# Kernel optimization log

Measured on AMD Instinct MI355X. Metric: run time of the kernel, lower is better.

## Reference

```python
import jax, jax.numpy as jnp
import numpy as np

B, SQ, SKV = 4, 4096, 1024
QDIM, CDIM = 1024, 768
HEADS, DHEAD = 16, 64
INNER = HEADS * DHEAD


def setup_inputs() -> dict:
    key = jax.random.key(0)
    ks = jax.random.split(key, 7)
    s = 0.02
    return {
        "x": jax.random.normal(ks[0], (B, SQ, QDIM), dtype=jnp.float32),
        "context": jax.random.normal(ks[1], (B, SKV, CDIM), dtype=jnp.float32),
        "Wq": jax.random.normal(ks[2], (QDIM, INNER), dtype=jnp.float32) * s,
        "Wk": jax.random.normal(ks[3], (CDIM, INNER), dtype=jnp.float32) * s,
        "Wv": jax.random.normal(ks[4], (CDIM, INNER), dtype=jnp.float32) * s,
        "Wo": jax.random.normal(ks[5], (INNER, QDIM), dtype=jnp.float32) * s,
        "bo": jnp.zeros((QDIM,), dtype=jnp.float32),
    }


def reference(x, context, Wq, Wk, Wv, Wo, bo):
    # QKV projections (no bias, matching bias=False Linear layers)
    q = x @ Wq          # [B, SQ, INNER]
    k = context @ Wk    # [B, SKV, INNER]
    v = context @ Wv    # [B, SKV, INNER]

    # split heads: b s (h d) -> b h s d
    def split_heads(t, s):
        return t.reshape(B, s, HEADS, DHEAD).transpose(0, 2, 1, 3)

    qh = split_heads(q, SQ)
    kh = split_heads(k, SKV)
    vh = split_heads(v, SKV)

    scale = DHEAD ** -0.5  # attention_basic default scale
    sim = jnp.einsum('bhqd,bhkd->bhqk', qh, kh) * scale  # [B,H,SQ,SKV]
    attn = jax.nn.softmax(sim, axis=-1)
    out = jnp.einsum('bhqk,bhkd->bhqd', attn, vh)        # [B,H,SQ,DHEAD]
    out = out.transpose(0, 2, 1, 3).reshape(B, SQ, INNER)

    # output projection (Linear with bias); dropout p=0 -> identity
    return out @ Wo + bo
```

## Files before the change

kernel.cpp:

```cpp
#include <hip/hip_runtime.h>


typedef unsigned short u16;
typedef unsigned int u32;
typedef __bf16 bf16x8 __attribute__((ext_vector_type(8)));
typedef float float4v __attribute__((ext_vector_type(4)));
typedef _Float16 half4 __attribute__((ext_vector_type(4)));
typedef _Float16 half2v __attribute__((ext_vector_type(2)));
typedef __attribute__((address_space(1))) void as1_void;
typedef __attribute__((address_space(3))) void as3_void;

__device__ __forceinline__ u16 f2bf(float f) {
  unsigned u = __float_as_uint(f);
  u += 0x7FFF + ((u >> 16) & 1);
  return (u16)(u >> 16);
}

__device__ __forceinline__ void async16(const u16* g, u16* l) {
  __builtin_amdgcn_global_load_lds((as1_void*)(void*)g, (as3_void*)l, 16, 0, 0);
}

#define WAITCNT_VM8 0xF78
#define WAITCNT_VM4 0xF74
#define WAITCNT_VM0 0xF70

__global__ void cvt_kernel(const float* __restrict__ x, u16* __restrict__ xbf,
                           const float* __restrict__ ctx, u16* __restrict__ ctxbf) {
  int i = blockIdx.x * 256 + threadIdx.x;
  const float* in; u16* out; int j;
  if (i < 4194304) { in = x; out = xbf; j = i; }
  else if (i < 4980736) { in = ctx; out = ctxbf; j = i - 4194304; }
  else return;
  float4 v = ((const float4*)in)[j];
  ushort4 o;
  o.x = f2bf(v.x); o.y = f2bf(v.y); o.z = f2bf(v.z); o.w = f2bf(v.w);
  ((ushort4*)out)[j] = o;
}

__global__ void twt_kernel(const float* __restrict__ Wq, const float* __restrict__ Wk,
                           const float* __restrict__ Wv, const float* __restrict__ Wo,
                           u16* __restrict__ WqT, u16* __restrict__ WkT,
                           u16* __restrict__ WvT, u16* __restrict__ WoT) {
  __shared__ u16 t[32][33];
  int z = blockIdx.z;
  const float* W = z == 0 ? Wq : z == 1 ? Wk : z == 2 ? Wv : Wo;
  u16* Wt = z == 0 ? WqT : z == 1 ? WkT : z == 2 ? WvT : WoT;
  int Kd = (z == 1 || z == 2) ? 768 : 1024;
  int k0 = blockIdx.y * 32;
  if (k0 >= Kd) return;
  int tx = threadIdx.x, ty = threadIdx.y;
  int n0 = blockIdx.x * 32;
#pragma unroll
  for (int i = 0; i < 4; i++)
    t[ty + i * 8][tx] = f2bf(W[(size_t)(k0 + ty + i * 8) * 1024 + n0 + tx]);
  __syncthreads();
#pragma unroll
  for (int i = 0; i < 4; i++)
    Wt[(size_t)(n0 + ty + i * 8) * Kd + k0 + tx] = t[tx][ty + i * 8];
}


__device__ __forceinline__ void ld_a4(const u16 (*Lp)[256][8], int rbase, int quad,
                                      int l15, bf16x8 a[4][2]) {
#pragma unroll
  for (int mi = 0; mi < 4; mi++)
#pragma unroll
    for (int ks = 0; ks < 2; ks++)
      a[mi][ks] = *(const bf16x8*)&Lp[ks * 4 + quad][rbase + mi * 16 + l15][0];
}

__device__ __forceinline__ void ld_b2(const u16 (*Lp)[256][8], int rbase, int quad,
                                      int l15, bf16x8 b[2][2]) {
#pragma unroll
  for (int ni = 0; ni < 2; ni++)
#pragma unroll
    for (int ks = 0; ks < 2; ks++)
      b[ni][ks] = *(const bf16x8*)&Lp[ks * 4 + quad][rbase + ni * 16 + l15][0];
}

__device__ __forceinline__ void mm16(bf16x8 a[4][2], bf16x8 b[2][2],
                                     float4v acc[8][4], int mh, int nh) {
  __builtin_amdgcn_s_setprio(1);
#pragma unroll
  for (int mi = 0; mi < 4; mi++)
#pragma unroll
    for (int ni = 0; ni < 2; ni++)
#pragma unroll
      for (int ks = 0; ks < 2; ks++)
        acc[mh * 4 + mi][nh * 2 + ni] = __builtin_amdgcn_mfma_f32_16x16x32_bf16(
            a[mi][ks], b[ni][ks], acc[mh * 4 + mi][nh * 2 + ni], 0, 0, 0);
  __builtin_amdgcn_s_setprio(0);
}

__device__ __forceinline__ void gemm256_core(const u16* __restrict__ A,
                                             const u16* __restrict__ Bt, int K,
                                             int m0, int n0, float4v acc[8][4]) {
  __shared__ __align__(16) u16 L[2][2][8][256][8];
  int tid = threadIdx.x;
  int w = tid >> 6, lane = tid & 63;
  int l15 = lane & 15, quad = lane >> 4;
  int wm = (w >> 2) * 128, wn = (w & 3) * 64;

  int c0 = 2 * w, c1 = 2 * w + 1;
  int kc0 = c0 & 7, mb0 = (c0 >> 3) * 64;
  int kc1 = c1 & 7, mb1 = (c1 >> 3) * 64;
  const u16* pA0 = A + (size_t)(m0 + mb0 + lane) * K + kc0 * 8;
  const u16* pA1 = A + (size_t)(m0 + mb1 + lane) * K + kc1 * 8;
  const u16* pB0 = Bt + (size_t)(n0 + mb0 + lane) * K + kc0 * 8;
  const u16* pB1 = Bt + (size_t)(n0 + mb1 + lane) * K + kc1 * 8;
  size_t hs = (size_t)128 * K;

#define STG_A(buf, t)                                                          \
  do {                                                                         \
    const u16* s0 = pA0 + (size_t)(t) * 64;                                    \
    const u16* s1 = pA1 + (size_t)(t) * 64;                                    \
    async16(s0, &L[buf][0][kc0][mb0][0]);                                      \
    async16(s1, &L[buf][0][kc1][mb1][0]);                                      \
    async16(s0 + hs, &L[buf][0][kc0][128 + mb0][0]);                           \
    async16(s1 + hs, &L[buf][0][kc1][128 + mb1][0]);                           \
  } while (0)
#define STG_B(buf, t)                                                          \
  do {                                                                         \
    const u16* s0 = pB0 + (size_t)(t) * 64;                                    \
    const u16* s1 = pB1 + (size_t)(t) * 64;                                    \
    async16(s0, &L[buf][1][kc0][mb0][0]);                                      \
    async16(s1, &L[buf][1][kc1][mb1][0]);                                      \
    async16(s0 + hs, &L[buf][1][kc0][128 + mb0][0]);                           \
    async16(s1 + hs, &L[buf][1][kc1][128 + mb1][0]);                           \
  } while (0)

  STG_A(0, 0); STG_B(0, 0);
  STG_A(1, 1); STG_B(1, 1);
  __builtin_amdgcn_s_waitcnt(WAITCNT_VM8);
  __builtin_amdgcn_s_barrier();

  bf16x8 a[4][2], b0[2][2], b1[2][2];
  int I = K >> 7;
  for (int i = 0; i < I; ++i) {
    int st = (i + 1 < I);
    ld_a4(L[0][0], wm, quad, l15, a);
    ld_b2(L[0][1], wn, quad, l15, b0);
    if (i > 0) STG_B(1, 2 * i + 1);
    __builtin_amdgcn_s_barrier();
    mm16(a, b0, acc, 0, 0);
    __builtin_amdgcn_s_barrier();
    ld_b2(L[0][1], wn + 32, quad, l15, b1);
    __builtin_amdgcn_s_barrier();
    mm16(a, b1, acc, 0, 1);
    __builtin_amdgcn_s_barrier();
    ld_a4(L[0][0], wm + 64, quad, l15, a);
    __builtin_amdgcn_s_barrier();
    mm16(a, b1, acc, 1, 1);
    __builtin_amdgcn_s_barrier();
    if (st) STG_A(0, 2 * i + 2);
    __builtin_amdgcn_s_barrier();
    mm16(a, b0, acc, 1, 0);
    if (st) __builtin_amdgcn_s_waitcnt(WAITCNT_VM4);
    else    __builtin_amdgcn_s_waitcnt(WAITCNT_VM0);
    __builtin_amdgcn_s_barrier();
    ld_a4(L[1][0], wm, quad, l15, a);
    ld_b2(L[1][1], wn, quad, l15, b0);
    if (st) STG_B(0, 2 * i + 2);
    __builtin_amdgcn_s_barrier();
    mm16(a, b0, acc, 0, 0);
    __builtin_amdgcn_s_barrier();
    ld_b2(L[1][1], wn + 32, quad, l15, b1);
    __builtin_amdgcn_s_barrier();
    mm16(a, b1, acc, 0, 1);
    __builtin_amdgcn_s_barrier();
    ld_a4(L[1][0], wm + 64, quad, l15, a);
    __builtin_amdgcn_s_barrier();
    mm16(a, b1, acc, 1, 1);
    __builtin_amdgcn_s_barrier();
    if (st) STG_A(1, 2 * i + 3);
    __builtin_amdgcn_s_barrier();
    mm16(a, b0, acc, 1, 0);
    if (st) __builtin_amdgcn_s_waitcnt(WAITCNT_VM4);
    __builtin_amdgcn_s_barrier();
  }
#undef STG_A
#undef STG_B
}

__global__ __launch_bounds__(512, 2) void qkv_gemm8(
    const u16* __restrict__ xbf, const u16* __restrict__ ctxbf,
    const u16* __restrict__ WqT, const u16* __restrict__ WkT, const u16* __restrict__ WvT,
    u16* __restrict__ Qb, u16* __restrict__ Kbuf, u16* __restrict__ Vtb, float qscale) {
  int bx = blockIdx.x;
  const u16* A; const u16* Bt; u16* C; int K, mode, m0, n0; float scale;
  if (bx < 256)      { int t = bx;       A = xbf;   Bt = WqT; C = Qb;   K = 1024; mode = 0; scale = qscale; m0 = (t >> 2) * 256; n0 = (t & 3) * 256; }
  else if (bx < 320) { int t = bx - 256; A = ctxbf; Bt = WkT; C = Kbuf; K = 768;  mode = 0; scale = 1.0f;   m0 = (t >> 2) * 256; n0 = (t & 3) * 256; }
  else               { int t = bx - 320; A = ctxbf; Bt = WvT; C = Vtb;  K = 768;  mode = 2; scale = 1.0f;   m0 = (t >> 2) * 256; n0 = (t & 3) * 256; }

  float4v acc[8][4] = {};
  gemm256_core(A, Bt, K, m0, n0, acc);

  int tid = threadIdx.x;
  int w = tid >> 6, lane = tid & 63;
  int l15 = lane & 15, quad = lane >> 4;
  int wm = (w >> 2) * 128, wn = (w & 3) * 64;

  if (mode == 0) {
#pragma unroll
    for (int mi = 0; mi < 8; mi++) {
      int rowb = m0 + wm + mi * 16 + quad * 4;
#pragma unroll
      for (int ni = 0; ni < 4; ni++) {
        int col = n0 + wn + ni * 16 + l15;
#pragma unroll
        for (int r = 0; r < 4; r++)
          C[(size_t)(rowb + r) * 1024 + col] = f2bf(acc[mi][ni][r] * scale);
      }
    }
  } else {
#pragma unroll
    for (int mi = 0; mi < 8; mi++) {
      int rowb = m0 + wm + mi * 16 + quad * 4;
#pragma unroll
      for (int ni = 0; ni < 4; ni++) {
        int col = n0 + wn + ni * 16 + l15;
        int hh = col >> 6, dd = col & 63;
#pragma unroll
        for (int r = 0; r < 4; r++) {
          int rr = rowb + r;
          int b = rr >> 10, skv = rr & 1023;
          _Float16 hv = (_Float16)acc[mi][ni][r];
          C[((((size_t)b * 16 + hh) * 64 + dd) << 10) + skv] = __builtin_bit_cast(u16, hv);
        }
      }
    }
  }
}

__global__ __launch_bounds__(512, 2) void gemm_bt8(
    const u16* __restrict__ A, const u16* __restrict__ Bt,
    float* __restrict__ C, const float* __restrict__ bias) {
  int bx = blockIdx.x;
  int m0 = (bx >> 2) * 256, n0 = (bx & 3) * 256;

  float4v acc[8][4] = {};
  gemm256_core(A, Bt, 1024, m0, n0, acc);

  int tid = threadIdx.x;
  int w = tid >> 6, lane = tid & 63;
  int l15 = lane & 15, quad = lane >> 4;
  int wm = (w >> 2) * 128, wn = (w & 3) * 64;

#pragma unroll
  for (int mi = 0; mi < 8; mi++) {
    int rowb = m0 + wm + mi * 16 + quad * 4;
#pragma unroll
    for (int ni = 0; ni < 4; ni++) {
      int col = n0 + wn + ni * 16 + l15;
      float bv = bias[col];
#pragma unroll
      for (int r = 0; r < 4; r++)
        C[(size_t)(rowb + r) * 1024 + col] = acc[mi][ni][r] + bv;
    }
  }
}

__global__ __launch_bounds__(512, 4) void attn_kernel(
    const u16* __restrict__ Q, const u16* __restrict__ Kb,
    const u16* __restrict__ Vt, u16* __restrict__ Oout) {
  __shared__ __align__(16) u16 lK[2][8192];
  __shared__ __align__(16) u16 lV[2][8192];
  int tid = threadIdx.x, w = tid >> 6, lane = tid & 63;
  int l15 = lane & 15, quad = lane >> 4;
  int bh = blockIdx.y, b = bh >> 4, h = bh & 15;
  int q0 = blockIdx.x * 256 + w * 32;

  const u16* Qbase = Q + ((size_t)(b * 4096 + q0)) * 1024 + h * 64;
  const u16* Kbase = Kb + ((size_t)b << 20) + h * 64;
  const u16* Vbase = Vt + ((size_t)bh << 16);

  bf16x8 qf[2][2];
#pragma unroll
  for (int qt = 0; qt < 2; qt++)
#pragma unroll
    for (int c = 0; c < 2; c++)
      qf[qt][c] = *(const bf16x8*)(Qbase + (size_t)(qt * 16 + l15) * 1024 + c * 32 + quad * 8);

  int kr0 = tid >> 3, kx0 = ((tid & 7) ^ (kr0 & 7)) * 8;
  const u16* ks0 = Kbase + (size_t)kr0 * 1024 + kx0;
  const u16* ks1 = ks0 + (size_t)64 * 1024;
  int vd0 = tid >> 4, vc0 = ((tid & 15) ^ (vd0 & 15)) * 8;
  const u16* vs0 = Vbase + (size_t)vd0 * 1024 + vc0;
  const u16* vs1 = vs0 + (size_t)32 * 1024;
  int kdo0 = w * 512, kdo1 = 4096 + w * 512;

  async16(ks0, &lK[0][kdo0]); async16(ks1, &lK[0][kdo1]);
  async16(vs0, &lV[0][kdo0]); async16(vs1, &lV[0][kdo1]);
  ks0 += 131072; ks1 += 131072;
  vs0 += 128; vs1 += 128;

  float4v o[2][4] = {};
  float4v osum[2] = {};
  const half4 ones = {(_Float16)1.0f, (_Float16)1.0f, (_Float16)1.0f, (_Float16)1.0f};

  int lb = l15 & 7;
  int xk0 = ((0 + quad) ^ lb) * 16 + l15 * 128;
  int xk1 = ((4 + quad) ^ lb) * 16 + l15 * 128;
  int qh = quad >> 1, qo = (quad & 1) * 8;
  int vrow = l15 * 256 + qo;

  for (int it = 0; it < 8; ++it) {
    const char* bK = (const char*)lK + (it & 1) * 16384;
    const char* bV = (const char*)lV + (it & 1) * 16384;
    __syncthreads();
    if (it < 7) {
      int nb = (it + 1) & 1;
      async16(ks0, &lK[nb][kdo0]); async16(ks1, &lK[nb][kdo1]);
      async16(vs0, &lV[nb][kdo0]); async16(vs1, &lV[nb][kdo1]);
      ks0 += 131072; ks1 += 131072;
      vs0 += 128; vs1 += 128;
    }
#pragma unroll
    for (int ss = 0; ss < 8; ss++) {
      int sub = (ss + w) & 7;
      int sb = sub * 2048;
      float4v sv[2] = {{0.f, 0.f, 0.f, 0.f}, {0.f, 0.f, 0.f, 0.f}};
      __builtin_amdgcn_s_setprio(1);
#pragma unroll
      for (int c = 0; c < 2; c++) {
        bf16x8 kf = *(const bf16x8*)(bK + sb + (c ? xk1 : xk0));
#pragma unroll
        for (int qt = 0; qt < 2; qt++)
          sv[qt] = __builtin_amdgcn_mfma_f32_16x16x32_bf16(kf, qf[qt][c], sv[qt], 0, 0, 0);
      }
      __builtin_amdgcn_s_setprio(0);
      half4 pf[2];
#pragma unroll
      for (int qt = 0; qt < 2; qt++) {
        float e0 = exp2f(sv[qt][0]), e1 = exp2f(sv[qt][1]);
        float e2 = exp2f(sv[qt][2]), e3 = exp2f(sv[qt][3]);
        half2v p01 = __builtin_bit_cast(half2v, __builtin_amdgcn_cvt_pkrtz(e0, e1));
        half2v p23 = __builtin_bit_cast(half2v, __builtin_amdgcn_cvt_pkrtz(e2, e3));
        pf[qt] = __builtin_shufflevector(p01, p23, 0, 1, 2, 3);
        osum[qt] = __builtin_amdgcn_mfma_f32_16x16x16f16(ones, pf[qt], osum[qt], 0, 0, 0);
      }
      int vbs = vrow + (((sub * 2 + qh) ^ l15) * 16);
      __builtin_amdgcn_s_setprio(1);
#pragma unroll
      for (int dt = 0; dt < 4; dt++) {
        half4 vf = *(const half4*)(bV + dt * 4096 + vbs);
#pragma unroll
        for (int qt = 0; qt < 2; qt++)
          o[qt][dt] = __builtin_amdgcn_mfma_f32_16x16x16f16(vf, pf[qt], o[qt][dt], 0, 0, 0);
      }
      __builtin_amdgcn_s_setprio(0);
    }
  }

#pragma unroll
  for (int qt = 0; qt < 2; qt++) {
    float inv = 1.0f / osum[qt][0];
    u16* Ob = Oout + ((size_t)(b * 4096 + q0 + qt * 16 + l15)) * 1024 + h * 64 + quad * 4;
#pragma unroll
    for (int dt = 0; dt < 4; dt++) {
      ushort4 pk;
      pk.x = f2bf(o[qt][dt][0] * inv);
      pk.y = f2bf(o[qt][dt][1] * inv);
      pk.z = f2bf(o[qt][dt][2] * inv);
      pk.w = f2bf(o[qt][dt][3] * inv);
      *(ushort4*)(Ob + dt * 16) = pk;
    }
  }
}

extern "C" void kernel_launch(void* const* d_in, const int* in_sizes, int n_in,
                              void* d_out, int out_size, void* d_ws, size_t ws_size,
                              hipStream_t stream) {
  const float* x   = (const float*)d_in[0];
  const float* ctx = (const float*)d_in[1];
  const float* Wq  = (const float*)d_in[2];
  const float* Wk  = (const float*)d_in[3];
  const float* Wv  = (const float*)d_in[4];
  const float* Wo  = (const float*)d_in[5];
  const float* bo  = (const float*)d_in[6];
  float* out = (float*)d_out;

  u16* ws    = (u16*)d_ws;
  u16* xbf   = ws;
  u16* ctxbf = xbf + 16777216;
  u16* WqT   = ctxbf + 3145728;
  u16* WkT   = WqT + 1048576;
  u16* WvT   = WkT + 786432;
  u16* WoT   = WvT + 786432;
  u16* Qb    = WoT + 1048576;
  u16* Kbuf  = Qb + 16777216;
  u16* Vtb   = Kbuf + 4194304;
  if (ws_size < (size_t)48758784 * 2) return;

  cvt_kernel<<<19456, 256, 0, stream>>>(x, xbf, ctx, ctxbf);
  twt_kernel<<<dim3(32, 32, 4), dim3(32, 8), 0, stream>>>(Wq, Wk, Wv, Wo, WqT, WkT, WvT, WoT);
  qkv_gemm8<<<dim3(384), dim3(512), 0, stream>>>(xbf, ctxbf, WqT, WkT, WvT,
                                                 Qb, Kbuf, Vtb, 0.18033688011112042f);
  attn_kernel<<<dim3(16, 64), dim3(512), 0, stream>>>(Qb, Kbuf, Vtb, xbf);
  gemm_bt8<<<dim3(256), dim3(512), 0, stream>>>(xbf, WoT, out, bo);
}
```

Before: 378.3 us.

## Replace 256x256 GEMM tiles with 128x128 triple-buffered tiles and block swizzle

Replaces the 8-wave 256x256 GEMM core, with its two-stage buffering and fine-grained barriers, by a 4-wave 128x128 core using three LDS stages with K=32 slices and one barrier per iteration. Block indices are remapped so that consecutive blocks are spread across XCD-style groups. More, smaller tiles should improve wave-level load balance and occupancy on 256 CUs (1536 and 1024 blocks instead of 384 and 256), at the cost of less operand reuse per tile and more global and LDS traffic. The unpadded [128][32] LDS layout may cause bank conflicts.

```diff
diff --git a/kernel.cpp b/kernel.cpp
--- a/kernel.cpp
+++ b/kernel.cpp
@@ -59,150 +59,86 @@
     Wt[(size_t)(n0 + ty + i * 8) * Kd + k0 + tx] = t[tx][ty + i * 8];
 }
 
-
-__device__ __forceinline__ void ld_a4(const u16 (*Lp)[256][8], int rbase, int quad,
-                                      int l15, bf16x8 a[4][2]) {
-#pragma unroll
-  for (int mi = 0; mi < 4; mi++)
-#pragma unroll
-    for (int ks = 0; ks < 2; ks++)
-      a[mi][ks] = *(const bf16x8*)&Lp[ks * 4 + quad][rbase + mi * 16 + l15][0];
-}
-
-__device__ __forceinline__ void ld_b2(const u16 (*Lp)[256][8], int rbase, int quad,
-                                      int l15, bf16x8 b[2][2]) {
-#pragma unroll
-  for (int ni = 0; ni < 2; ni++)
-#pragma unroll
-    for (int ks = 0; ks < 2; ks++)
-      b[ni][ks] = *(const bf16x8*)&Lp[ks * 4 + quad][rbase + ni * 16 + l15][0];
-}
-
-__device__ __forceinline__ void mm16(bf16x8 a[4][2], bf16x8 b[2][2],
-                                     float4v acc[8][4], int mh, int nh) {
-  __builtin_amdgcn_s_setprio(1);
-#pragma unroll
-  for (int mi = 0; mi < 4; mi++)
-#pragma unroll
-    for (int ni = 0; ni < 2; ni++)
-#pragma unroll
-      for (int ks = 0; ks < 2; ks++)
-        acc[mh * 4 + mi][nh * 2 + ni] = __builtin_amdgcn_mfma_f32_16x16x32_bf16(
-            a[mi][ks], b[ni][ks], acc[mh * 4 + mi][nh * 2 + ni], 0, 0, 0);
-  __builtin_amdgcn_s_setprio(0);
-}
-
-__device__ __forceinline__ void gemm256_core(const u16* __restrict__ A,
+__device__ __forceinline__ void gemm128_core(const u16* __restrict__ A,
                                              const u16* __restrict__ Bt, int K,
-                                             int m0, int n0, float4v acc[8][4]) {
-  __shared__ __align__(16) u16 L[2][2][8][256][8];
+                                             int m0, int n0, float4v acc[4][4]) {
+  __shared__ __align__(16) u16 L[3][2][128][32];
   int tid = threadIdx.x;
   int w = tid >> 6, lane = tid & 63;
   int l15 = lane & 15, quad = lane >> 4;
-  int wm = (w >> 2) * 128, wn = (w & 3) * 64;
-
-  int c0 = 2 * w, c1 = 2 * w + 1;
-  int kc0 = c0 & 7, mb0 = (c0 >> 3) * 64;
-  int kc1 = c1 & 7, mb1 = (c1 >> 3) * 64;
-  const u16* pA0 = A + (size_t)(m0 + mb0 + lane) * K + kc0 * 8;
-  const u16* pA1 = A + (size_t)(m0 + mb1 + lane) * K + kc1 * 8;
-  const u16* pB0 = Bt + (size_t)(n0 + mb0 + lane) * K + kc0 * 8;
-  const u16* pB1 = Bt + (size_t)(n0 + mb1 + lane) * K + kc1 * 8;
-  size_t hs = (size_t)128 * K;
-
-#define STG_A(buf, t)                                                          \
+  int wm = (w >> 1) * 64, wn = (w & 1) * 64;
+
+  const u16* pA = A + (size_t)(m0 + (tid >> 2)) * K + (tid & 3) * 8;
+  const u16* pB = Bt + (size_t)(n0 + (tid >> 2)) * K + (tid & 3) * 8;
+  size_t r64 = (size_t)64 * K;
+  int dofs = tid * 8;
+
+#define STG(buf, t)                                                            \
   do {                                                                         \
-    const u16* s0 = pA0 + (size_t)(t) * 64;                                    \
-    const u16* s1 = pA1 + (size_t)(t) * 64;                                    \
-    async16(s0, &L[buf][0][kc0][mb0][0]);                                      \
-    async16(s1, &L[buf][0][kc1][mb1][0]);                                      \
-    async16(s0 + hs, &L[buf][0][kc0][128 + mb0][0]);                           \
-    async16(s1 + hs, &L[buf][0][kc1][128 + mb1][0]);                           \
+    const u16* sa = pA + (size_t)(t) * 32;                                     \
+    const u16* sb = pB + (size_t)(t) * 32;                                     \
+    async16(sa, &L[buf][0][0][0] + dofs);                                      \
+    async16(sa + r64, &L[buf][0][0][0] + dofs + 2048);                         \
+    async16(sb, &L[buf][1][0][0] + dofs);                                      \
+    async16(sb + r64, &L[buf][1][0][0] + dofs + 2048);                         \
   } while (0)
-#define STG_B(buf, t)                                                          \
-  do {                                                                         \
-    const u16* s0 = pB0 + (size_t)(t) * 64;                                    \
-    const u16* s1 = pB1 + (size_t)(t) * 64;                                    \
-    async16(s0, &L[buf][1][kc0][mb0][0]);                                      \
-    async16(s1, &L[buf][1][kc1][mb1][0]);                                      \
-    async16(s0 + hs, &L[buf][1][kc0][128 + mb0][0]);                           \
-    async16(s1 + hs, &L[buf][1][kc1][128 + mb1][0]);                           \
-  } while (0)
-
-  STG_A(0, 0); STG_B(0, 0);
-  STG_A(1, 1); STG_B(1, 1);
-  __builtin_amdgcn_s_waitcnt(WAITCNT_VM8);
-  __builtin_amdgcn_s_barrier();
-
-  bf16x8 a[4][2], b0[2][2], b1[2][2];
-  int I = K >> 7;
-  for (int i = 0; i < I; ++i) {
-    int st = (i + 1 < I);
-    ld_a4(L[0][0], wm, quad, l15, a);
-    ld_b2(L[0][1], wn, quad, l15, b0);
-    if (i > 0) STG_B(1, 2 * i + 1);
+
+  STG(0, 0);
+  STG(1, 1);
+
+  int niter = K >> 5;
+  int cb = 0;
+  for (int it = 0; it < niter; ++it) {
+    if (it + 1 < niter) __builtin_amdgcn_s_waitcnt(WAITCNT_VM4);
+    else                __builtin_amdgcn_s_waitcnt(WAITCNT_VM0);
     __builtin_amdgcn_s_barrier();
-    mm16(a, b0, acc, 0, 0);
-    __builtin_amdgcn_s_barrier();
-    ld_b2(L[0][1], wn + 32, quad, l15, b1);
-    __builtin_amdgcn_s_barrier();
-    mm16(a, b1, acc, 0, 1);
-    __builtin_amdgcn_s_barrier();
-    ld_a4(L[0][0], wm + 64, quad, l15, a);
-    __builtin_amdgcn_s_barrier();
-    mm16(a, b1, acc, 1, 1);
-    __builtin_amdgcn_s_barrier();
-    if (st) STG_A(0, 2 * i + 2);
-    __builtin_amdgcn_s_barrier();
-    mm16(a, b0, acc, 1, 0);
-    if (st) __builtin_amdgcn_s_waitcnt(WAITCNT_VM4);
-    else    __builtin_amdgcn_s_waitcnt(WAITCNT_VM0);
-    __builtin_amdgcn_s_barrier();
-    ld_a4(L[1][0], wm, quad, l15, a);
-    ld_b2(L[1][1], wn, quad, l15, b0);
-    if (st) STG_B(0, 2 * i + 2);
-    __builtin_amdgcn_s_barrier();
-    mm16(a, b0, acc, 0, 0);
-    __builtin_amdgcn_s_barrier();
-    ld_b2(L[1][1], wn + 32, quad, l15, b1);
-    __builtin_amdgcn_s_barrier();
-    mm16(a, b1, acc, 0, 1);
-    __builtin_amdgcn_s_barrier();
-    ld_a4(L[1][0], wm + 64, quad, l15, a);
-    __builtin_amdgcn_s_barrier();
-    mm16(a, b1, acc, 1, 1);
-    __builtin_amdgcn_s_barrier();
-    if (st) STG_A(1, 2 * i + 3);
-    __builtin_amdgcn_s_barrier();
-    mm16(a, b0, acc, 1, 0);
-    if (st) __builtin_amdgcn_s_waitcnt(WAITCNT_VM4);
-    __builtin_amdgcn_s_barrier();
-  }
-#undef STG_A
-#undef STG_B
-}
-
-__global__ __launch_bounds__(512, 2) void qkv_gemm8(
+    if (it + 2 < niter) {
+      int pb = cb + 2; if (pb >= 3) pb -= 3;
+      STG(pb, it + 2);
+    }
+    const u16* cA = &L[cb][0][0][0];
+    const u16* cB = &L[cb][1][0][0];
+    bf16x8 fa[4], fb[4];
+#pragma unroll
+    for (int mi = 0; mi < 4; mi++)
+      fa[mi] = *(const bf16x8*)&cA[(wm + mi * 16 + l15) * 32 + quad * 8];
+#pragma unroll
+    for (int ni = 0; ni < 4; ni++)
+      fb[ni] = *(const bf16x8*)&cB[(wn + ni * 16 + l15) * 32 + quad * 8];
+    __builtin_amdgcn_s_setprio(1);
+#pragma unroll
+    for (int mi = 0; mi < 4; mi++)
+#pragma unroll
+      for (int ni = 0; ni < 4; ni++)
+        acc[mi][ni] = __builtin_amdgcn_mfma_f32_16x16x32_bf16(fa[mi], fb[ni], acc[mi][ni], 0, 0, 0);
+    __builtin_amdgcn_s_setprio(0);
+    cb = (cb + 1 == 3) ? 0 : cb + 1;
+  }
+#undef STG
+}
+
+__global__ __launch_bounds__(256, 3) void qkv_gemm128(
     const u16* __restrict__ xbf, const u16* __restrict__ ctxbf,
     const u16* __restrict__ WqT, const u16* __restrict__ WkT, const u16* __restrict__ WvT,
     u16* __restrict__ Qb, u16* __restrict__ Kbuf, u16* __restrict__ Vtb, float qscale) {
-  int bx = blockIdx.x;
+  int bx0 = blockIdx.x;
+  int bx = (bx0 & 7) * 192 + (bx0 >> 3);
   const u16* A; const u16* Bt; u16* C; int K, mode, m0, n0; float scale;
-  if (bx < 256)      { int t = bx;       A = xbf;   Bt = WqT; C = Qb;   K = 1024; mode = 0; scale = qscale; m0 = (t >> 2) * 256; n0 = (t & 3) * 256; }
-  else if (bx < 320) { int t = bx - 256; A = ctxbf; Bt = WkT; C = Kbuf; K = 768;  mode = 0; scale = 1.0f;   m0 = (t >> 2) * 256; n0 = (t & 3) * 256; }
-  else               { int t = bx - 320; A = ctxbf; Bt = WvT; C = Vtb;  K = 768;  mode = 2; scale = 1.0f;   m0 = (t >> 2) * 256; n0 = (t & 3) * 256; }
-
-  float4v acc[8][4] = {};
-  gemm256_core(A, Bt, K, m0, n0, acc);
+  if (bx < 1024)      { int t = bx;        A = xbf;   Bt = WqT; C = Qb;   K = 1024; mode = 0; scale = qscale; m0 = (t >> 3) * 128; n0 = (t & 7) * 128; }
+  else if (bx < 1280) { int t = bx - 1024; A = ctxbf; Bt = WkT; C = Kbuf; K = 768;  mode = 0; scale = 1.0f;   m0 = (t >> 3) * 128; n0 = (t & 7) * 128; }
+  else                { int t = bx - 1280; A = ctxbf; Bt = WvT; C = Vtb;  K = 768;  mode = 2; scale = 1.0f;   m0 = (t >> 3) * 128; n0 = (t & 7) * 128; }
+
+  float4v acc[4][4] = {};
+  gemm128_core(A, Bt, K, m0, n0, acc);
 
   int tid = threadIdx.x;
   int w = tid >> 6, lane = tid & 63;
   int l15 = lane & 15, quad = lane >> 4;
-  int wm = (w >> 2) * 128, wn = (w & 3) * 64;
+  int wm = (w >> 1) * 64, wn = (w & 1) * 64;
 
   if (mode == 0) {
 #pragma unroll
-    for (int mi = 0; mi < 8; mi++) {
+    for (int mi = 0; mi < 4; mi++) {
       int rowb = m0 + wm + mi * 16 + quad * 4;
 #pragma unroll
       for (int ni = 0; ni < 4; ni++) {
@@ -214,7 +150,7 @@
     }
   } else {
 #pragma unroll
-    for (int mi = 0; mi < 8; mi++) {
+    for (int mi = 0; mi < 4; mi++) {
       int rowb = m0 + wm + mi * 16 + quad * 4;
 #pragma unroll
       for (int ni = 0; ni < 4; ni++) {
@@ -232,22 +168,23 @@
   }
 }
 
-__global__ __launch_bounds__(512, 2) void gemm_bt8(
+__global__ __launch_bounds__(256, 3) void gemm_bt128(
     const u16* __restrict__ A, const u16* __restrict__ Bt,
     float* __restrict__ C, const float* __restrict__ bias) {
-  int bx = blockIdx.x;
-  int m0 = (bx >> 2) * 256, n0 = (bx & 3) * 256;
-
-  float4v acc[8][4] = {};
-  gemm256_core(A, Bt, 1024, m0, n0, acc);
+  int bx0 = blockIdx.x;
+  int bx = (bx0 & 7) * 128 + (bx0 >> 3);
+  int m0 = (bx >> 3) * 128, n0 = (bx & 7) * 128;
+
+  float4v acc[4][4] = {};
+  gemm128_core(A, Bt, 1024, m0, n0, acc);
 
   int tid = threadIdx.x;
   int w = tid >> 6, lane = tid & 63;
   int l15 = lane & 15, quad = lane >> 4;
-  int wm = (w >> 2) * 128, wn = (w & 3) * 64;
-
-#pragma unroll
-  for (int mi = 0; mi < 8; mi++) {
+  int wm = (w >> 1) * 64, wn = (w & 1) * 64;
+
+#pragma unroll
+  for (int mi = 0; mi < 4; mi++) {
     int rowb = m0 + wm + mi * 16 + quad * 4;
 #pragma unroll
     for (int ni = 0; ni < 4; ni++) {
@@ -394,8 +331,8 @@
 
   cvt_kernel<<<19456, 256, 0, stream>>>(x, xbf, ctx, ctxbf);
   twt_kernel<<<dim3(32, 32, 4), dim3(32, 8), 0, stream>>>(Wq, Wk, Wv, Wo, WqT, WkT, WvT, WoT);
-  qkv_gemm8<<<dim3(384), dim3(512), 0, stream>>>(xbf, ctxbf, WqT, WkT, WvT,
-                                                 Qb, Kbuf, Vtb, 0.18033688011112042f);
+  qkv_gemm128<<<dim3(1536), dim3(256), 0, stream>>>(xbf, ctxbf, WqT, WkT, WvT,
+                                                    Qb, Kbuf, Vtb, 0.18033688011112042f);
   attn_kernel<<<dim3(16, 64), dim3(512), 0, stream>>>(Qb, Kbuf, Vtb, xbf);
-  gemm_bt8<<<dim3(256), dim3(512), 0, stream>>>(xbf, WoT, out, bo);
-}
+  gemm_bt128<<<dim3(1024), dim3(256), 0, stream>>>(xbf, WoT, out, bo);
+}
```

Result: faster. 346.9 us (-8.3%).
